# Performance work log

Measured on AMD Instinct MI355X. Metric: run time of the kernel, lower is better.

The kernel has to match this reference:

```python
import jax, jax.numpy as jnp
import numpy as np
from jax.ops import segment_sum

N_NODES = 100000

def setup_inputs() -> dict:
    key = jax.random.key(0)
    k1, k2, k3 = jax.random.split(key, 3)
    x = jax.random.normal(k1, (N_NODES, 128), dtype=jnp.float32)
    edge_weight = jax.random.uniform(k2, (3200000,), dtype=jnp.float32)
    edge_index = jax.random.randint(k3, (2, 3200000), 0, N_NODES, dtype=jnp.int64)
    return {"x": x, "edge_weight": edge_weight, "edge_index": edge_index}

def reference(x, edge_weight, edge_index):
    # GCNConv with weight forced to identity (in==out channels, no bias):
    # lin(x) == x, so the op is gcn_norm + scatter-add aggregation.
    n = x.shape[0]
    # add self loops with fill value 1.0 (improved=False)
    loop_idx = jnp.arange(n, dtype=edge_index.dtype)
    row = jnp.concatenate([edge_index[0], loop_idx])
    col = jnp.concatenate([edge_index[1], loop_idx])
    ew = jnp.concatenate([edge_weight, jnp.ones((n,), dtype=edge_weight.dtype)])
    # symmetric normalization: deg computed at target (col)
    deg = segment_sum(ew, col, num_segments=n)
    dinv = jnp.where(deg > 0, jax.lax.rsqrt(deg), 0.0)
    norm = dinv[row] * ew * dinv[col]
    # message = norm * x[src]; aggregate (sum) at target
    msgs = x[row] * norm[:, None]          # [E+N, d]
    out = segment_sum(msgs, col, num_segments=n)  # [N, d]
    return out
```

## Files before the change

kernel.cpp:

```cpp
#include <hip/hip_runtime.h>
#include <hip/hip_fp16.h>
#include <math.h>

#define FEAT      128
#define PITCH     72
#define CH        6144
#define K_EDGES   12
#define MAXBINS   512
#define STAGE_CAP 9216
#define K2        18

__global__ void conv_xs_kernel(const float* __restrict__ x,
                               const float* __restrict__ deg,
                               __half2* __restrict__ xs, int n4) {
    int i = blockIdx.x * blockDim.x + threadIdx.x;
    if (i >= n4) return;
    float s = rsqrtf(1.0f + deg[i >> 5]);
    float4 v = ((const float4*)x)[i];
    xs[2 * i]     = __floats2half2_rn(s * v.x, s * v.y);
    xs[2 * i + 1] = __floats2half2_rn(s * v.z, s * v.w);
}

__global__ __launch_bounds__(512) void p1_partition_kernel(
        const int* __restrict__ row,
        const int* __restrict__ col,
        const float* __restrict__ ew,
        int* __restrict__ bin_cursor,
        unsigned long long* __restrict__ binned,
        int E, int NBINS, int cap) {
    __shared__ unsigned long long stage[CH];
    __shared__ int hist[MAXBINS];
    __shared__ int lofs[MAXBINS];
    __shared__ int lcnt[MAXBINS];
    __shared__ int gbase[MAXBINS];
    __shared__ int scanbuf[MAXBINS];
    int tid = threadIdx.x;
    if (tid < MAXBINS) { hist[tid] = 0; lcnt[tid] = 0; }
    __syncthreads();

    int start = blockIdx.x * CH;
    int end   = start + CH; if (end > E) end = E;
    int total = end - start;

    unsigned long long ed[K_EDGES];
    int ebin[K_EDGES];
    #pragma unroll
    for (int k = 0; k < K_EDGES; k++) {
        int e = start + (k << 9) + tid;
        if (e < end) {
            int c = col[e];
            unsigned short wh = __half_as_ushort(__float2half_rn(ew[e]));
            ed[k] = ((unsigned long long)wh << 48)
                  | ((unsigned long long)((unsigned)row[e] & 0xFFFFFFu) << 24)
                  | (unsigned)(c & 0xFFFFFFu);
            ebin[k] = c >> 8;
            atomicAdd(&hist[ebin[k]], 1);
        } else {
            ebin[k] = -1;
        }
    }
    __syncthreads();

    int h = (tid < NBINS) ? hist[tid] : 0;
    scanbuf[tid] = h;
    __syncthreads();
    #pragma unroll
    for (int off = 1; off < MAXBINS; off <<= 1) {
        int t = (tid >= off) ? scanbuf[tid - off] : 0;
        __syncthreads();
        scanbuf[tid] += t;
        __syncthreads();
    }
    lofs[tid] = scanbuf[tid] - h;
    __syncthreads();

    #pragma unroll
    for (int k = 0; k < K_EDGES; k++) {
        if (ebin[k] >= 0) {
            int pos = lofs[ebin[k]] + atomicAdd(&lcnt[ebin[k]], 1);
            stage[pos] = ed[k];
        }
    }
    if (tid < NBINS)
        gbase[tid] = hist[tid] ? atomicAdd(&bin_cursor[tid], hist[tid]) : 0;
    __syncthreads();

    for (int i = tid; i < total; i += 512) {
        unsigned long long e = stage[i];
        int bin = (int)((e >> 8) & 0xFFFFu);
        int pos = gbase[bin] + (i - lofs[bin]);
        if (pos < cap) binned[(size_t)bin * cap + pos] = e;
    }
}

__global__ __launch_bounds__(512) void p2_build_kernel(
        const unsigned long long* __restrict__ binned,
        int* __restrict__ bin_cursor,
        unsigned long long* __restrict__ csr,
        float* __restrict__ deg,
        int* __restrict__ countg,
        int N, int NBINS, int cap) {
    __shared__ unsigned long long stage[STAGE_CAP];
    __shared__ float degf[256];
    __shared__ int cnt[256];
    __shared__ int pfx[256];
    __shared__ int lcnt[256];
    __shared__ int wsum[4];
    __shared__ int binBase_s;
    int tid = threadIdx.x;
    if (tid < 256) { degf[tid] = 0.0f; cnt[tid] = 0; lcnt[tid] = 0; }
    __syncthreads();

    int b = blockIdx.x;
    int nE = bin_cursor[b]; if (nE > cap) nE = cap;
    const unsigned long long* src = binned + (size_t)b * cap;
    int nodeBase = b << 8;

    unsigned long long ed[K2];
    #pragma unroll
    for (int k = 0; k < K2; k++) {
        int i = tid + (k << 9);
        if (i < nE) {
            unsigned long long p = src[i];
            int cl     = (int)(p & 255u);
            unsigned r = (unsigned)((p >> 24) & 0xFFFFFFu);
            float w = __half2float(__ushort_as_half((unsigned short)(p >> 48)));
            atomicAdd(&cnt[cl], 1);
            atomicAdd(&degf[cl], w);
            ed[k] = ((unsigned long long)__float_as_uint(w) << 32)
                  | ((unsigned)cl << 24) | r;
        }
    }
    if (tid == 0) binBase_s = atomicAdd(&bin_cursor[NBINS], nE);
    __syncthreads();

    if (tid < 256) {
        int w = tid >> 6, l = tid & 63;
        int v = cnt[tid];
        int inc = v;
        #pragma unroll
        for (int d = 1; d < 64; d <<= 1) {
            int t = __shfl_up(inc, d);
            if (l >= d) inc += t;
        }
        if (l == 63) wsum[w] = inc;
        pfx[tid] = inc - v;
    }
    __syncthreads();
    if (tid < 256) {
        int w = tid >> 6;
        int add = 0;
        for (int q = 0; q < w; q++) add += wsum[q];
        pfx[tid] += add;
    }
    __syncthreads();

    #pragma unroll
    for (int k = 0; k < K2; k++) {
        int i = tid + (k << 9);
        if (i < nE) {
            unsigned long long p = ed[k];
            int cl = (int)((p >> 24) & 255u);
            int slot = atomicAdd(&lcnt[cl], 1);
            stage[pfx[cl] + slot] = p & 0xFFFFFFFF00FFFFFFULL;
        }
    }
    __syncthreads();

    int binBase = binBase_s;
    for (int i = tid; i < nE; i += 512)
        csr[(size_t)binBase + i] = stage[i];
    if (tid < 256) {
        int node = nodeBase + tid;
        if (node < N) {
            deg[node] = degf[tid];
            int c2 = cnt[tid]; if (c2 > 255) c2 = 255;
            countg[node] = (int)((((unsigned)(binBase + pfx[tid])) << 8) | (unsigned)c2);
        }
    }
}

__global__ __launch_bounds__(256) void gather_xs_kernel(
        const __half2* __restrict__ xs,
        const float* __restrict__ deg,
        const int* __restrict__ countg,
        const unsigned long long* __restrict__ csr,
        float* __restrict__ out, int n) {
    __shared__ unsigned long long eb[4][64];
    int wid  = threadIdx.x >> 6;
    int node = blockIdx.x * 4 + wid;
    int lane = threadIdx.x & 63;
    if (node >= n) return;

    float di = rsqrtf(1.0f + deg[node]);
    unsigned c = (unsigned)countg[node];
    int cnt = (int)(c & 255u);
    const unsigned long long* b = csr + (c >> 8);

    unsigned long long e0 = (lane < cnt) ? b[lane] : 0ULL;
    eb[wid][lane] = e0;

    unsigned xbase = ((unsigned)node << 6) | (unsigned)lane;
    float2 xv = __half22float2(xs[xbase]);
    float2 a0 = xv;
    float2 a1 = {0.f, 0.f}, a2 = {0.f, 0.f}, a3 = {0.f, 0.f};

    int m = cnt < 64 ? cnt : 64;
    int j = 0;
    for (; j + 8 <= m; j += 8) {
        unsigned long long p0 = eb[wid][j + 0];
        unsigned long long p1 = eb[wid][j + 1];
        unsigned long long p2 = eb[wid][j + 2];
        unsigned long long p3 = eb[wid][j + 3];
        unsigned long long p4 = eb[wid][j + 4];
        unsigned long long p5 = eb[wid][j + 5];
        unsigned long long p6 = eb[wid][j + 6];
        unsigned long long p7 = eb[wid][j + 7];
        unsigned r0 = (unsigned)p0, r1 = (unsigned)p1, r2 = (unsigned)p2, r3 = (unsigned)p3;
        unsigned r4 = (unsigned)p4, r5 = (unsigned)p5, r6 = (unsigned)p6, r7 = (unsigned)p7;
        float w0 = __uint_as_float((unsigned)(p0 >> 32));
        float w1 = __uint_as_float((unsigned)(p1 >> 32));
        float w2 = __uint_as_float((unsigned)(p2 >> 32));
        float w3 = __uint_as_float((unsigned)(p3 >> 32));
        float w4 = __uint_as_float((unsigned)(p4 >> 32));
        float w5 = __uint_as_float((unsigned)(p5 >> 32));
        float w6 = __uint_as_float((unsigned)(p6 >> 32));
        float w7 = __uint_as_float((unsigned)(p7 >> 32));
        float2 v0 = __half22float2(xs[(r0 << 6) | lane]);
        float2 v1 = __half22float2(xs[(r1 << 6) | lane]);
        float2 v2 = __half22float2(xs[(r2 << 6) | lane]);
        float2 v3 = __half22float2(xs[(r3 << 6) | lane]);
        float2 v4 = __half22float2(xs[(r4 << 6) | lane]);
        float2 v5 = __half22float2(xs[(r5 << 6) | lane]);
        float2 v6 = __half22float2(xs[(r6 << 6) | lane]);
        float2 v7 = __half22float2(xs[(r7 << 6) | lane]);
        a0.x = fmaf(w0, v0.x, a0.x);  a0.y = fmaf(w0, v0.y, a0.y);
        a1.x = fmaf(w1, v1.x, a1.x);  a1.y = fmaf(w1, v1.y, a1.y);
        a2.x = fmaf(w2, v2.x, a2.x);  a2.y = fmaf(w2, v2.y, a2.y);
        a3.x = fmaf(w3, v3.x, a3.x);  a3.y = fmaf(w3, v3.y, a3.y);
        a0.x = fmaf(w4, v4.x, a0.x);  a0.y = fmaf(w4, v4.y, a0.y);
        a1.x = fmaf(w5, v5.x, a1.x);  a1.y = fmaf(w5, v5.y, a1.y);
        a2.x = fmaf(w6, v6.x, a2.x);  a2.y = fmaf(w6, v6.y, a2.y);
        a3.x = fmaf(w7, v7.x, a3.x);  a3.y = fmaf(w7, v7.y, a3.y);
    }
    for (; j + 4 <= m; j += 4) {
        unsigned long long p0 = eb[wid][j + 0];
        unsigned long long p1 = eb[wid][j + 1];
        unsigned long long p2 = eb[wid][j + 2];
        unsigned long long p3 = eb[wid][j + 3];
        unsigned r0 = (unsigned)p0, r1 = (unsigned)p1, r2 = (unsigned)p2, r3 = (unsigned)p3;
        float w0 = __uint_as_float((unsigned)(p0 >> 32));
        float w1 = __uint_as_float((unsigned)(p1 >> 32));
        float w2 = __uint_as_float((unsigned)(p2 >> 32));
        float w3 = __uint_as_float((unsigned)(p3 >> 32));
        float2 v0 = __half22float2(xs[(r0 << 6) | lane]);
        float2 v1 = __half22float2(xs[(r1 << 6) | lane]);
        float2 v2 = __half22float2(xs[(r2 << 6) | lane]);
        float2 v3 = __half22float2(xs[(r3 << 6) | lane]);
        a0.x = fmaf(w0, v0.x, a0.x);  a0.y = fmaf(w0, v0.y, a0.y);
        a1.x = fmaf(w1, v1.x, a1.x);  a1.y = fmaf(w1, v1.y, a1.y);
        a2.x = fmaf(w2, v2.x, a2.x);  a2.y = fmaf(w2, v2.y, a2.y);
        a3.x = fmaf(w3, v3.x, a3.x);  a3.y = fmaf(w3, v3.y, a3.y);
    }
    for (; j < m; ++j) {
        unsigned long long p0 = eb[wid][j];
        unsigned r0 = (unsigned)p0;
        float w0 = __uint_as_float((unsigned)(p0 >> 32));
        float2 v0 = __half22float2(xs[(r0 << 6) | lane]);
        a0.x = fmaf(w0, v0.x, a0.x);  a0.y = fmaf(w0, v0.y, a0.y);
    }
    for (; j < cnt; ++j) {
        unsigned long long p0 = b[j];
        unsigned r0 = (unsigned)p0;
        float w0 = __uint_as_float((unsigned)(p0 >> 32));
        float2 v0 = __half22float2(xs[(r0 << 6) | lane]);
        a0.x = fmaf(w0, v0.x, a0.x);  a0.y = fmaf(w0, v0.y, a0.y);
    }
    float2 r;
    r.x = di * ((a0.x + a1.x) + (a2.x + a3.x));
    r.y = di * ((a0.y + a1.y) + (a2.y + a3.y));
    ((float2*)(out + (size_t)node * FEAT))[lane] = r;
}


__global__ void init_packed_kernel(unsigned long long* __restrict__ packed, int n) {
    int i = blockIdx.x * blockDim.x + threadIdx.x;
    if (i < n) packed[i] = (1ULL << 32);
}

__global__ void passA_kernel(const int* __restrict__ row,
                             const int* __restrict__ col,
                             const float* __restrict__ ew,
                             unsigned long long* __restrict__ packed,
                             unsigned long long* __restrict__ bucket, int E) {
    int e = blockIdx.x * blockDim.x + threadIdx.x;
    if (e >= E) return;
    int c = col[e], r = row[e];
    float w = ew[e];
    unsigned long long v = (1ULL << 40)
        | (unsigned long long)((double)w * 4294967296.0);
    unsigned long long old = atomicAdd(&packed[c], v);
    unsigned int slot = (unsigned int)(old >> 40);
    if (slot < PITCH)
        bucket[(size_t)c * PITCH + slot] =
            ((unsigned long long)__float_as_uint(w) << 32) | ((unsigned int)r & 0xFFFFFFu);
}

__global__ void make_deg_count_kernel(const unsigned long long* __restrict__ packed,
                                      float* __restrict__ deg,
                                      int* __restrict__ countg, int n) {
    int i = blockIdx.x * blockDim.x + threadIdx.x;
    if (i < n) {
        unsigned long long p = packed[i];
        unsigned long long frac = p & ((1ULL << 40) - 1);
        float d = (float)((double)frac * (1.0 / 4294967296.0));
        deg[i] = d - 1.0f;
        int c = (int)(p >> 40); if (c > PITCH) c = PITCH;
        countg[i] = (int)((((unsigned)i * (unsigned)PITCH) << 8) | (unsigned)c);
    }
}


__global__ void init_deg_kernel(float* __restrict__ deg, int n) {
    int i = blockIdx.x * blockDim.x + threadIdx.x;
    if (i < n) deg[i] = 1.0f;
}
__global__ void deg_accum_kernel(const int* __restrict__ col,
                                 const float* __restrict__ ew,
                                 float* __restrict__ deg, int E) {
    int e = blockIdx.x * blockDim.x + threadIdx.x;
    if (e < E) atomicAdd(&deg[col[e]], ew[e]);
}
__global__ void make_dinv_kernel(const float* __restrict__ deg,
                                 float* __restrict__ dinv, int n) {
    int i = blockIdx.x * blockDim.x + threadIdx.x;
    if (i < n) {
        float d = deg[i];
        dinv[i] = d > 0.0f ? rsqrtf(d) : 0.0f;
    }
}
__global__ void init_out_kernel(const float* __restrict__ x,
                                const float* __restrict__ dinv,
                                float* __restrict__ out, int n) {
    int idx = blockIdx.x * blockDim.x + threadIdx.x;
    int i = idx >> 5, lane = idx & 31;
    if (i >= n) return;
    float s = dinv[i] * dinv[i];
    float4 v = ((const float4*)(x + (size_t)i * FEAT))[lane];
    float4 r;
    r.x = s * v.x; r.y = s * v.y; r.z = s * v.z; r.w = s * v.w;
    ((float4*)(out + (size_t)i * FEAT))[lane] = r;
}
__global__ void scatter_kernel(const float* __restrict__ x,
                               const float* __restrict__ ew,
                               const int* __restrict__ row,
                               const int* __restrict__ col,
                               const float* __restrict__ dinv,
                               float* __restrict__ out, int E) {
    long long idx = (long long)blockIdx.x * blockDim.x + threadIdx.x;
    int e = (int)(idx >> 5), lane = (int)(idx & 31);
    if (e >= E) return;
    int r = row[e], c = col[e];
    float nrm = dinv[r] * ew[e] * dinv[c];
    float4 v = ((const float4*)(x + (size_t)r * FEAT))[lane];
    float* o = out + (size_t)c * FEAT + lane * 4;
    atomicAdd(o + 0, nrm * v.x);
    atomicAdd(o + 1, nrm * v.y);
    atomicAdd(o + 2, nrm * v.z);
    atomicAdd(o + 3, nrm * v.w);
}


static inline size_t align256(size_t v) { return (v + 255) & ~(size_t)255; }

extern "C" void kernel_launch(void* const* d_in, const int* in_sizes, int n_in,
                              void* d_out, int out_size, void* d_ws, size_t ws_size,
                              hipStream_t stream) {
    const float* x  = (const float*)d_in[0];
    const float* ew = (const float*)d_in[1];
    const int*   ei = (const int*)d_in[2];

    const int N = in_sizes[0] / FEAT;
    const int E = in_sizes[1];
    const int* row = ei;
    const int* col = ei + E;

    float* out = (float*)d_out;
    const int B = 256;
    char* w = (char*)d_ws;

    const int NBINS = (N + 255) >> 8;
    const int avg   = (E + NBINS - 1) / NBINS;
    int cap = avg + 8 * (int)sqrt((double)avg) + 64;
    if (cap > STAGE_CAP) cap = STAGE_CAP;

    size_t sz_csr    = align256((size_t)E * 8 + 256);
    size_t sz_bucket = align256((size_t)N * PITCH * 8);
    size_t sz_deg    = align256((size_t)N * 4);
    size_t sz_count  = align256((size_t)N * 4);
    size_t sz_cursor = align256((size_t)(NBINS + 1) * 4);
    size_t sz_binned = align256((size_t)NBINS * (size_t)cap * 8);
    size_t sz_xs     = align256((size_t)N * FEAT * 2);
    size_t sz_shared = sz_binned > sz_xs ? sz_binned : sz_xs;

    size_t need_fast2 = sz_csr + sz_deg + sz_count + sz_cursor + sz_shared;
    size_t need_fast1 = align256((size_t)N * 8) + sz_deg + sz_count + sz_xs + sz_bucket;

    int nodes_per_block = B / 64;
    int gblocks = (N + nodes_per_block - 1) / nodes_per_block;
    int n4 = N * FEAT / 4;

    if (ws_size >= need_fast2 && NBINS <= MAXBINS && N < (1 << 24) && E < (1 << 24)) {
        unsigned long long* csr = (unsigned long long*)w;     w += sz_csr;
        float* deg    = (float*)w;                            w += sz_deg;
        int*   countg = (int*)w;                              w += sz_count;
        int*   cursor = (int*)w;                              w += sz_cursor;
        unsigned long long* binned = (unsigned long long*)w;
        __half2* xs = (__half2*)binned;

        hipMemsetAsync(cursor, 0, (size_t)(NBINS + 1) * 4, stream);
        int p1b = (E + CH - 1) / CH;
        p1_partition_kernel<<<p1b, 512, 0, stream>>>(row, col, ew, cursor, binned,
                                                     E, NBINS, cap);
        p2_build_kernel<<<NBINS, 512, 0, stream>>>(binned, cursor, csr,
                                                   deg, countg, N, NBINS, cap);
        conv_xs_kernel<<<(n4 + B - 1) / B, B, 0, stream>>>(x, deg, xs, n4);
        gather_xs_kernel<<<gblocks, B, 0, stream>>>(xs, deg, countg, csr, out, N);
    } else if (ws_size >= need_fast1 && N < (1 << 24) &&
               (size_t)N * PITCH < (size_t)(1 << 24)) {
        unsigned long long* packed = (unsigned long long*)w;  w += align256((size_t)N * 8);
        float*   deg    = (float*)w;                          w += sz_deg;
        int*     countg = (int*)w;                            w += sz_count;
        __half2* xs     = (__half2*)w;                        w += sz_xs;
        unsigned long long* bucket = (unsigned long long*)w;

        init_packed_kernel<<<(N + B - 1) / B, B, 0, stream>>>(packed, N);
        passA_kernel<<<(E + B - 1) / B, B, 0, stream>>>(row, col, ew, packed, bucket, E);
        make_deg_count_kernel<<<(N + B - 1) / B, B, 0, stream>>>(packed, deg, countg, N);
        conv_xs_kernel<<<(n4 + B - 1) / B, B, 0, stream>>>(x, deg, xs, n4);
        gather_xs_kernel<<<gblocks, B, 0, stream>>>(xs, deg, countg, bucket, out, N);
    } else {
        float* deg  = (float*)w;                  w += sz_deg;
        float* dinv = (float*)w;
        init_deg_kernel<<<(N + B - 1) / B, B, 0, stream>>>(deg, N);
        deg_accum_kernel<<<(E + B - 1) / B, B, 0, stream>>>(col, ew, deg, E);
        make_dinv_kernel<<<(N + B - 1) / B, B, 0, stream>>>(deg, dinv, N);
        long long it = (long long)N * 32;
        init_out_kernel<<<(int)((it + B - 1) / B), B, 0, stream>>>(x, dinv, out, N);
        long long st = (long long)E * 32;
        scatter_kernel<<<(int)((st + B - 1) / B), B, 0, stream>>>(x, ew, row, col, dinv, out, E);
    }
}
```

Baseline: 295.0 us.

## Drop shared staging in partition/build and fuse feature conversion into build

The partition kernel no longer sorts edges through a shared-memory stage with a block-wide scan. Each edge now takes its slot from one shared atomic and is written straight to its global bin position. The build kernel likewise scatters edges straight into CSR and drops its large shared stage. It also computes dinv once and does the x-to-half scaling itself, which removes the separate conversion kernel. The trade is less shared memory per block and fewer launches against uncoalesced global scatter writes. The half-precision feature buffer now needs its own workspace region instead of reusing the binned buffer.

```diff
diff --git a/kernel.cpp b/kernel.cpp
--- a/kernel.cpp
+++ b/kernel.cpp
@@ -7,15 +7,15 @@
 #define CH        6144
 #define K_EDGES   12
 #define MAXBINS   512
-#define STAGE_CAP 9216
+#define CAP_MAX   9216
 #define K2        18
 
 __global__ void conv_xs_kernel(const float* __restrict__ x,
-                               const float* __restrict__ deg,
+                               const float* __restrict__ dinv,
                                __half2* __restrict__ xs, int n4) {
     int i = blockIdx.x * blockDim.x + threadIdx.x;
     if (i >= n4) return;
-    float s = rsqrtf(1.0f + deg[i >> 5]);
+    float s = dinv[i >> 5];
     float4 v = ((const float4*)x)[i];
     xs[2 * i]     = __floats2half2_rn(s * v.x, s * v.y);
     xs[2 * i + 1] = __floats2half2_rn(s * v.z, s * v.w);
@@ -28,68 +28,47 @@
         int* __restrict__ bin_cursor,
         unsigned long long* __restrict__ binned,
         int E, int NBINS, int cap) {
-    __shared__ unsigned long long stage[CH];
-    __shared__ int hist[MAXBINS];
-    __shared__ int lofs[MAXBINS];
     __shared__ int lcnt[MAXBINS];
     __shared__ int gbase[MAXBINS];
-    __shared__ int scanbuf[MAXBINS];
     int tid = threadIdx.x;
-    if (tid < MAXBINS) { hist[tid] = 0; lcnt[tid] = 0; }
+    if (tid < MAXBINS) lcnt[tid] = 0;
     __syncthreads();
 
     int start = blockIdx.x * CH;
     int end   = start + CH; if (end > E) end = E;
-    int total = end - start;
 
     unsigned long long ed[K_EDGES];
-    int ebin[K_EDGES];
+    int meta[K_EDGES];
     #pragma unroll
     for (int k = 0; k < K_EDGES; k++) {
         int e = start + (k << 9) + tid;
+        meta[k] = -1;
         if (e < end) {
             int c = col[e];
             unsigned short wh = __half_as_ushort(__float2half_rn(ew[e]));
             ed[k] = ((unsigned long long)wh << 48)
                   | ((unsigned long long)((unsigned)row[e] & 0xFFFFFFu) << 24)
                   | (unsigned)(c & 0xFFFFFFu);
-            ebin[k] = c >> 8;
-            atomicAdd(&hist[ebin[k]], 1);
-        } else {
-            ebin[k] = -1;
-        }
-    }
-    __syncthreads();
-
-    int h = (tid < NBINS) ? hist[tid] : 0;
-    scanbuf[tid] = h;
-    __syncthreads();
-    #pragma unroll
-    for (int off = 1; off < MAXBINS; off <<= 1) {
-        int t = (tid >= off) ? scanbuf[tid - off] : 0;
-        __syncthreads();
-        scanbuf[tid] += t;
-        __syncthreads();
-    }
-    lofs[tid] = scanbuf[tid] - h;
+            int bin = c >> 8;
+            int slot = atomicAdd(&lcnt[bin], 1);
+            meta[k] = (slot << 16) | bin;
+        }
+    }
+    __syncthreads();
+
+    if (tid < NBINS) {
+        int h = lcnt[tid];
+        gbase[tid] = h ? atomicAdd(&bin_cursor[tid], h) : 0;
+    }
     __syncthreads();
 
     #pragma unroll
     for (int k = 0; k < K_EDGES; k++) {
-        if (ebin[k] >= 0) {
-            int pos = lofs[ebin[k]] + atomicAdd(&lcnt[ebin[k]], 1);
-            stage[pos] = ed[k];
-        }
-    }
-    if (tid < NBINS)
-        gbase[tid] = hist[tid] ? atomicAdd(&bin_cursor[tid], hist[tid]) : 0;
-    __syncthreads();
-
-    for (int i = tid; i < total; i += 512) {
-        unsigned long long e = stage[i];
-        int bin = (int)((e >> 8) & 0xFFFFu);
-        int pos = gbase[bin] + (i - lofs[bin]);
-        if (pos < cap) binned[(size_t)bin * cap + pos] = e;
+        if (meta[k] >= 0) {
+            int bin = meta[k] & 0xFFFF;
+            int pos = gbase[bin] + (meta[k] >> 16);
+            if (pos < cap) binned[(size_t)bin * cap + pos] = ed[k];
+        }
     }
 }
 
@@ -97,18 +76,19 @@
         const unsigned long long* __restrict__ binned,
         int* __restrict__ bin_cursor,
         unsigned long long* __restrict__ csr,
-        float* __restrict__ deg,
+        float* __restrict__ dinv,
         int* __restrict__ countg,
+        const float* __restrict__ x,
+        __half2* __restrict__ xs,
         int N, int NBINS, int cap) {
-    __shared__ unsigned long long stage[STAGE_CAP];
     __shared__ float degf[256];
     __shared__ int cnt[256];
     __shared__ int pfx[256];
-    __shared__ int lcnt[256];
+    __shared__ float sdi[256];
     __shared__ int wsum[4];
     __shared__ int binBase_s;
     int tid = threadIdx.x;
-    if (tid < 256) { degf[tid] = 0.0f; cnt[tid] = 0; lcnt[tid] = 0; }
+    if (tid < 256) { degf[tid] = 0.0f; cnt[tid] = 0; }
     __syncthreads();
 
     int b = blockIdx.x;
@@ -117,18 +97,20 @@
     int nodeBase = b << 8;
 
     unsigned long long ed[K2];
+    int meta[K2];
     #pragma unroll
     for (int k = 0; k < K2; k++) {
         int i = tid + (k << 9);
+        meta[k] = -1;
         if (i < nE) {
             unsigned long long p = src[i];
             int cl     = (int)(p & 255u);
             unsigned r = (unsigned)((p >> 24) & 0xFFFFFFu);
             float w = __half2float(__ushort_as_half((unsigned short)(p >> 48)));
-            atomicAdd(&cnt[cl], 1);
+            int slot = atomicAdd(&cnt[cl], 1);
             atomicAdd(&degf[cl], w);
-            ed[k] = ((unsigned long long)__float_as_uint(w) << 32)
-                  | ((unsigned)cl << 24) | r;
+            ed[k] = ((unsigned long long)__float_as_uint(w) << 32) | r;
+            meta[k] = (slot << 8) | cl;
         }
     }
     if (tid == 0) binBase_s = atomicAdd(&bin_cursor[NBINS], nE);
@@ -155,34 +137,46 @@
     }
     __syncthreads();
 
+    int binBase = binBase_s;
     #pragma unroll
     for (int k = 0; k < K2; k++) {
-        int i = tid + (k << 9);
-        if (i < nE) {
-            unsigned long long p = ed[k];
-            int cl = (int)((p >> 24) & 255u);
-            int slot = atomicAdd(&lcnt[cl], 1);
-            stage[pfx[cl] + slot] = p & 0xFFFFFFFF00FFFFFFULL;
-        }
-    }
-    __syncthreads();
-
-    int binBase = binBase_s;
-    for (int i = tid; i < nE; i += 512)
-        csr[(size_t)binBase + i] = stage[i];
+        if (meta[k] >= 0) {
+            int cl = meta[k] & 255;
+            csr[(size_t)binBase + pfx[cl] + (meta[k] >> 8)] = ed[k];
+        }
+    }
+
     if (tid < 256) {
         int node = nodeBase + tid;
         if (node < N) {
-            deg[node] = degf[tid];
+            float di = rsqrtf(1.0f + degf[tid]);
+            sdi[tid] = di;
+            dinv[node] = di;
             int c2 = cnt[tid]; if (c2 > 255) c2 = 255;
             countg[node] = (int)((((unsigned)(binBase + pfx[tid])) << 8) | (unsigned)c2);
+        } else {
+            sdi[tid] = 0.0f;
+        }
+    }
+    __syncthreads();
+
+    int nValid = N - nodeBase; if (nValid > 256) nValid = 256;
+    if (nValid > 0) {
+        int total4 = nValid << 5;
+        for (int idx = tid; idx < total4; idx += 512) {
+            int cl = idx >> 5;
+            float s = sdi[cl];
+            size_t g = ((size_t)(nodeBase + cl) << 5) + (idx & 31);
+            float4 v = ((const float4*)x)[g];
+            xs[2 * g]     = __floats2half2_rn(s * v.x, s * v.y);
+            xs[2 * g + 1] = __floats2half2_rn(s * v.z, s * v.w);
         }
     }
 }
 
 __global__ __launch_bounds__(256) void gather_xs_kernel(
         const __half2* __restrict__ xs,
-        const float* __restrict__ deg,
+        const float* __restrict__ dinv,
         const int* __restrict__ countg,
         const unsigned long long* __restrict__ csr,
         float* __restrict__ out, int n) {
@@ -192,7 +186,7 @@
     int lane = threadIdx.x & 63;
     if (node >= n) return;
 
-    float di = rsqrtf(1.0f + deg[node]);
+    float di = dinv[node];
     unsigned c = (unsigned)countg[node];
     int cnt = (int)(c & 255u);
     const unsigned long long* b = csr + (c >> 8);
@@ -306,15 +300,15 @@
             ((unsigned long long)__float_as_uint(w) << 32) | ((unsigned int)r & 0xFFFFFFu);
 }
 
-__global__ void make_deg_count_kernel(const unsigned long long* __restrict__ packed,
-                                      float* __restrict__ deg,
-                                      int* __restrict__ countg, int n) {
+__global__ void make_dinv_count_kernel(const unsigned long long* __restrict__ packed,
+                                       float* __restrict__ dinv,
+                                       int* __restrict__ countg, int n) {
     int i = blockIdx.x * blockDim.x + threadIdx.x;
     if (i < n) {
         unsigned long long p = packed[i];
         unsigned long long frac = p & ((1ULL << 40) - 1);
         float d = (float)((double)frac * (1.0 / 4294967296.0));
-        deg[i] = d - 1.0f;
+        dinv[i] = rsqrtf(d);
         int c = (int)(p >> 40); if (c > PITCH) c = PITCH;
         countg[i] = (int)((((unsigned)i * (unsigned)PITCH) << 8) | (unsigned)c);
     }
@@ -392,19 +386,18 @@
     const int NBINS = (N + 255) >> 8;
     const int avg   = (E + NBINS - 1) / NBINS;
     int cap = avg + 8 * (int)sqrt((double)avg) + 64;
-    if (cap > STAGE_CAP) cap = STAGE_CAP;
+    if (cap > CAP_MAX) cap = CAP_MAX;
 
     size_t sz_csr    = align256((size_t)E * 8 + 256);
     size_t sz_bucket = align256((size_t)N * PITCH * 8);
-    size_t sz_deg    = align256((size_t)N * 4);
+    size_t sz_dinv   = align256((size_t)N * 4);
     size_t sz_count  = align256((size_t)N * 4);
     size_t sz_cursor = align256((size_t)(NBINS + 1) * 4);
     size_t sz_binned = align256((size_t)NBINS * (size_t)cap * 8);
     size_t sz_xs     = align256((size_t)N * FEAT * 2);
-    size_t sz_shared = sz_binned > sz_xs ? sz_binned : sz_xs;
-
-    size_t need_fast2 = sz_csr + sz_deg + sz_count + sz_cursor + sz_shared;
-    size_t need_fast1 = align256((size_t)N * 8) + sz_deg + sz_count + sz_xs + sz_bucket;
+
+    size_t need_fast2 = sz_csr + sz_dinv + sz_count + sz_cursor + sz_binned + sz_xs;
+    size_t need_fast1 = align256((size_t)N * 8) + sz_dinv + sz_count + sz_xs + sz_bucket;
 
     int nodes_per_block = B / 64;
     int gblocks = (N + nodes_per_block - 1) / nodes_per_block;
@@ -412,35 +405,34 @@
 
     if (ws_size >= need_fast2 && NBINS <= MAXBINS && N < (1 << 24) && E < (1 << 24)) {
         unsigned long long* csr = (unsigned long long*)w;     w += sz_csr;
-        float* deg    = (float*)w;                            w += sz_deg;
+        float* dinv   = (float*)w;                            w += sz_dinv;
         int*   countg = (int*)w;                              w += sz_count;
         int*   cursor = (int*)w;                              w += sz_cursor;
-        unsigned long long* binned = (unsigned long long*)w;
-        __half2* xs = (__half2*)binned;
+        unsigned long long* binned = (unsigned long long*)w;  w += sz_binned;
+        __half2* xs = (__half2*)w;
 
         hipMemsetAsync(cursor, 0, (size_t)(NBINS + 1) * 4, stream);
         int p1b = (E + CH - 1) / CH;
         p1_partition_kernel<<<p1b, 512, 0, stream>>>(row, col, ew, cursor, binned,
                                                      E, NBINS, cap);
         p2_build_kernel<<<NBINS, 512, 0, stream>>>(binned, cursor, csr,
-                                                   deg, countg, N, NBINS, cap);
-        conv_xs_kernel<<<(n4 + B - 1) / B, B, 0, stream>>>(x, deg, xs, n4);
-        gather_xs_kernel<<<gblocks, B, 0, stream>>>(xs, deg, countg, csr, out, N);
+                                                   dinv, countg, x, xs, N, NBINS, cap);
+        gather_xs_kernel<<<gblocks, B, 0, stream>>>(xs, dinv, countg, csr, out, N);
     } else if (ws_size >= need_fast1 && N < (1 << 24) &&
                (size_t)N * PITCH < (size_t)(1 << 24)) {
         unsigned long long* packed = (unsigned long long*)w;  w += align256((size_t)N * 8);
-        float*   deg    = (float*)w;                          w += sz_deg;
+        float*   dinv   = (float*)w;                          w += sz_dinv;
         int*     countg = (int*)w;                            w += sz_count;
         __half2* xs     = (__half2*)w;                        w += sz_xs;
         unsigned long long* bucket = (unsigned long long*)w;
 
         init_packed_kernel<<<(N + B - 1) / B, B, 0, stream>>>(packed, N);
         passA_kernel<<<(E + B - 1) / B, B, 0, stream>>>(row, col, ew, packed, bucket, E);
-        make_deg_count_kernel<<<(N + B - 1) / B, B, 0, stream>>>(packed, deg, countg, N);
-        conv_xs_kernel<<<(n4 + B - 1) / B, B, 0, stream>>>(x, deg, xs, n4);
-        gather_xs_kernel<<<gblocks, B, 0, stream>>>(xs, deg, countg, bucket, out, N);
+        make_dinv_count_kernel<<<(N + B - 1) / B, B, 0, stream>>>(packed, dinv, countg, N);
+        conv_xs_kernel<<<(n4 + B - 1) / B, B, 0, stream>>>(x, dinv, xs, n4);
+        gather_xs_kernel<<<gblocks, B, 0, stream>>>(xs, dinv, countg, bucket, out, N);
     } else {
-        float* deg  = (float*)w;                  w += sz_deg;
+        float* deg  = (float*)w;                  w += sz_dinv;
         float* dinv = (float*)w;
         init_deg_kernel<<<(N + B - 1) / B, B, 0, stream>>>(deg, N);
         deg_accum_kernel<<<(E + B - 1) / B, B, 0, stream>>>(col, ew, deg, E);
```

Measured after the change: 305.5 us. +3.6%, slower.

## Fuse xs conversion into CSR build kernel and split gather launch

Applied to the files above, without the earlier changes.

The CSR build kernel now computes dinv per node (rsqrt once) and writes the dinv-scaled half-precision copy of x for its 256-node bin directly, removing the separate conversion kernel launch and the deg re-read. Because xs is written during p2, it can no longer alias the binned buffer, so the workspace layout gives xs its own region and needs more memory. The gather is split into two launches over node halves, which looks like a probe or an attempt to improve tail behaviour but adds a launch. Gather and conversion read precomputed dinv instead of recomputing rsqrt.

```diff
diff --git a/kernel.cpp b/kernel.cpp
--- a/kernel.cpp
+++ b/kernel.cpp
@@ -7,15 +7,15 @@
 #define CH        6144
 #define K_EDGES   12
 #define MAXBINS   512
-#define STAGE_CAP 9216
+#define CAP_MAX   9216
 #define K2        18
 
 __global__ void conv_xs_kernel(const float* __restrict__ x,
-                               const float* __restrict__ deg,
+                               const float* __restrict__ dinv,
                                __half2* __restrict__ xs, int n4) {
     int i = blockIdx.x * blockDim.x + threadIdx.x;
     if (i >= n4) return;
-    float s = rsqrtf(1.0f + deg[i >> 5]);
+    float s = dinv[i >> 5];
     float4 v = ((const float4*)x)[i];
     xs[2 * i]     = __floats2half2_rn(s * v.x, s * v.y);
     xs[2 * i + 1] = __floats2half2_rn(s * v.z, s * v.w);
@@ -97,14 +97,17 @@
         const unsigned long long* __restrict__ binned,
         int* __restrict__ bin_cursor,
         unsigned long long* __restrict__ csr,
-        float* __restrict__ deg,
+        float* __restrict__ dinv,
         int* __restrict__ countg,
+        const float* __restrict__ x,
+        __half2* __restrict__ xs,
         int N, int NBINS, int cap) {
-    __shared__ unsigned long long stage[STAGE_CAP];
+    __shared__ unsigned long long stage[CAP_MAX];
     __shared__ float degf[256];
     __shared__ int cnt[256];
     __shared__ int pfx[256];
     __shared__ int lcnt[256];
+    __shared__ float sdi[256];
     __shared__ int wsum[4];
     __shared__ int binBase_s;
     int tid = threadIdx.x;
@@ -173,26 +176,44 @@
     if (tid < 256) {
         int node = nodeBase + tid;
         if (node < N) {
-            deg[node] = degf[tid];
+            float di = rsqrtf(1.0f + degf[tid]);
+            sdi[tid] = di;
+            dinv[node] = di;
             int c2 = cnt[tid]; if (c2 > 255) c2 = 255;
             countg[node] = (int)((((unsigned)(binBase + pfx[tid])) << 8) | (unsigned)c2);
+        } else {
+            sdi[tid] = 0.0f;
+        }
+    }
+    __syncthreads();
+
+    int nValid = N - nodeBase; if (nValid > 256) nValid = 256;
+    if (nValid > 0) {
+        int total4 = nValid << 5;
+        for (int idx = tid; idx < total4; idx += 512) {
+            int cl = idx >> 5;
+            float s = sdi[cl];
+            size_t g = ((size_t)(nodeBase + cl) << 5) + (idx & 31);
+            float4 v = ((const float4*)x)[g];
+            xs[2 * g]     = __floats2half2_rn(s * v.x, s * v.y);
+            xs[2 * g + 1] = __floats2half2_rn(s * v.z, s * v.w);
         }
     }
 }
 
 __global__ __launch_bounds__(256) void gather_xs_kernel(
         const __half2* __restrict__ xs,
-        const float* __restrict__ deg,
+        const float* __restrict__ dinv,
         const int* __restrict__ countg,
         const unsigned long long* __restrict__ csr,
-        float* __restrict__ out, int n) {
+        float* __restrict__ out, int nodeBase, int nEnd) {
     __shared__ unsigned long long eb[4][64];
     int wid  = threadIdx.x >> 6;
-    int node = blockIdx.x * 4 + wid;
+    int node = nodeBase + blockIdx.x * 4 + wid;
     int lane = threadIdx.x & 63;
-    if (node >= n) return;
-
-    float di = rsqrtf(1.0f + deg[node]);
+    if (node >= nEnd) return;
+
+    float di = dinv[node];
     unsigned c = (unsigned)countg[node];
     int cnt = (int)(c & 255u);
     const unsigned long long* b = csr + (c >> 8);
@@ -306,15 +327,15 @@
             ((unsigned long long)__float_as_uint(w) << 32) | ((unsigned int)r & 0xFFFFFFu);
 }
 
-__global__ void make_deg_count_kernel(const unsigned long long* __restrict__ packed,
-                                      float* __restrict__ deg,
-                                      int* __restrict__ countg, int n) {
+__global__ void make_dinv_count_kernel(const unsigned long long* __restrict__ packed,
+                                       float* __restrict__ dinv,
+                                       int* __restrict__ countg, int n) {
     int i = blockIdx.x * blockDim.x + threadIdx.x;
     if (i < n) {
         unsigned long long p = packed[i];
         unsigned long long frac = p & ((1ULL << 40) - 1);
         float d = (float)((double)frac * (1.0 / 4294967296.0));
-        deg[i] = d - 1.0f;
+        dinv[i] = rsqrtf(d);
         int c = (int)(p >> 40); if (c > PITCH) c = PITCH;
         countg[i] = (int)((((unsigned)i * (unsigned)PITCH) << 8) | (unsigned)c);
     }
@@ -392,55 +413,53 @@
     const int NBINS = (N + 255) >> 8;
     const int avg   = (E + NBINS - 1) / NBINS;
     int cap = avg + 8 * (int)sqrt((double)avg) + 64;
-    if (cap > STAGE_CAP) cap = STAGE_CAP;
+    if (cap > CAP_MAX) cap = CAP_MAX;
 
     size_t sz_csr    = align256((size_t)E * 8 + 256);
     size_t sz_bucket = align256((size_t)N * PITCH * 8);
-    size_t sz_deg    = align256((size_t)N * 4);
+    size_t sz_dinv   = align256((size_t)N * 4);
     size_t sz_count  = align256((size_t)N * 4);
     size_t sz_cursor = align256((size_t)(NBINS + 1) * 4);
     size_t sz_binned = align256((size_t)NBINS * (size_t)cap * 8);
     size_t sz_xs     = align256((size_t)N * FEAT * 2);
-    size_t sz_shared = sz_binned > sz_xs ? sz_binned : sz_xs;
-
-    size_t need_fast2 = sz_csr + sz_deg + sz_count + sz_cursor + sz_shared;
-    size_t need_fast1 = align256((size_t)N * 8) + sz_deg + sz_count + sz_xs + sz_bucket;
-
-    int nodes_per_block = B / 64;
-    int gblocks = (N + nodes_per_block - 1) / nodes_per_block;
+
+    size_t need_fast2 = sz_csr + sz_dinv + sz_count + sz_cursor + sz_binned + sz_xs;
+    size_t need_fast1 = align256((size_t)N * 8) + sz_dinv + sz_count + sz_xs + sz_bucket;
+
     int n4 = N * FEAT / 4;
 
     if (ws_size >= need_fast2 && NBINS <= MAXBINS && N < (1 << 24) && E < (1 << 24)) {
         unsigned long long* csr = (unsigned long long*)w;     w += sz_csr;
-        float* deg    = (float*)w;                            w += sz_deg;
+        float* dinv   = (float*)w;                            w += sz_dinv;
         int*   countg = (int*)w;                              w += sz_count;
         int*   cursor = (int*)w;                              w += sz_cursor;
-        unsigned long long* binned = (unsigned long long*)w;
-        __half2* xs = (__half2*)binned;
+        unsigned long long* binned = (unsigned long long*)w;  w += sz_binned;
+        __half2* xs = (__half2*)w;
 
         hipMemsetAsync(cursor, 0, (size_t)(NBINS + 1) * 4, stream);
         int p1b = (E + CH - 1) / CH;
         p1_partition_kernel<<<p1b, 512, 0, stream>>>(row, col, ew, cursor, binned,
                                                      E, NBINS, cap);
         p2_build_kernel<<<NBINS, 512, 0, stream>>>(binned, cursor, csr,
-                                                   deg, countg, N, NBINS, cap);
-        conv_xs_kernel<<<(n4 + B - 1) / B, B, 0, stream>>>(x, deg, xs, n4);
-        gather_xs_kernel<<<gblocks, B, 0, stream>>>(xs, deg, countg, csr, out, N);
+                                                   dinv, countg, x, xs, N, NBINS, cap);
+        int H = ((N / 2) + 3) & ~3;
+        gather_xs_kernel<<<(H + 3) / 4, B, 0, stream>>>(xs, dinv, countg, csr, out, 0, H);
+        gather_xs_kernel<<<(N - H + 3) / 4, B, 0, stream>>>(xs, dinv, countg, csr, out, H, N);
     } else if (ws_size >= need_fast1 && N < (1 << 24) &&
                (size_t)N * PITCH < (size_t)(1 << 24)) {
         unsigned long long* packed = (unsigned long long*)w;  w += align256((size_t)N * 8);
-        float*   deg    = (float*)w;                          w += sz_deg;
+        float*   dinv   = (float*)w;                          w += sz_dinv;
         int*     countg = (int*)w;                            w += sz_count;
         __half2* xs     = (__half2*)w;                        w += sz_xs;
         unsigned long long* bucket = (unsigned long long*)w;
 
         init_packed_kernel<<<(N + B - 1) / B, B, 0, stream>>>(packed, N);
         passA_kernel<<<(E + B - 1) / B, B, 0, stream>>>(row, col, ew, packed, bucket, E);
-        make_deg_count_kernel<<<(N + B - 1) / B, B, 0, stream>>>(packed, deg, countg, N);
-        conv_xs_kernel<<<(n4 + B - 1) / B, B, 0, stream>>>(x, deg, xs, n4);
-        gather_xs_kernel<<<gblocks, B, 0, stream>>>(xs, deg, countg, bucket, out, N);
+        make_dinv_count_kernel<<<(N + B - 1) / B, B, 0, stream>>>(packed, dinv, countg, N);
+        conv_xs_kernel<<<(n4 + B - 1) / B, B, 0, stream>>>(x, dinv, xs, n4);
+        gather_xs_kernel<<<(N + 3) / 4, B, 0, stream>>>(xs, dinv, countg, bucket, out, 0, N);
     } else {
-        float* deg  = (float*)w;                  w += sz_deg;
+        float* deg  = (float*)w;                  w += sz_dinv;
         float* dinv = (float*)w;
         init_deg_kernel<<<(N + B - 1) / B, B, 0, stream>>>(deg, N);
         deg_accum_kernel<<<(E + B - 1) / B, B, 0, stream>>>(col, ew, deg, E);
```

New measurement: 297.3 us. Within noise of the previous version (+0.8%).
